# Kernel optimization log

Measured on AMD Instinct MI355X. Metric: run time of the kernel, lower is better.

## Reference

```python
import jax, jax.numpy as jnp
import numpy as np

EMBED_DIM = 1024
NUM_HEADS = 16
HEAD_DIM = EMBED_DIM // NUM_HEADS


def setup_inputs() -> dict:
    key = jax.random.key(0)
    k1, k2, k3, k4 = jax.random.split(key, 4)
    B, T, C = 4, 2048, EMBED_DIM
    scale = 1.0 / np.sqrt(C)
    x = jax.random.normal(k1, (B, T, C), dtype=jnp.float32)
    # nn.Linear(C, 3C, bias=False): weight [3C, C]
    w_qkv = jax.random.normal(k2, (3 * C, C), dtype=jnp.float32) * scale
    # nn.Linear(C, C) with bias
    w_out = jax.random.normal(k3, (C, C), dtype=jnp.float32) * scale
    b_out = jax.random.normal(k4, (C,), dtype=jnp.float32) * 0.01
    return {"x": x, "w_qkv": w_qkv, "w_out": w_out, "b_out": b_out}


def reference(x, w_qkv, w_out, b_out):
    B, T, C = x.shape
    H, D = NUM_HEADS, HEAD_DIM
    qkv = x @ w_qkv.T                      # [B,T,3C]
    q, k, v = jnp.split(qkv, 3, axis=-1)
    # [B,T,C] -> [B,H,T,D]
    q = q.reshape(B, T, H, D).transpose(0, 2, 1, 3)
    k = k.reshape(B, T, H, D).transpose(0, 2, 1, 3)
    v = v.reshape(B, T, H, D).transpose(0, 2, 1, 3)
    scores = jnp.einsum("bhqd,bhkd->bhqk", q, k) / jnp.sqrt(jnp.float32(D))
    causal = jnp.tril(jnp.ones((T, T), dtype=bool))
    scores = jnp.where(causal, scores, -jnp.inf)
    attn = jax.nn.softmax(scores, axis=-1)  # dropout is identity in eval mode
    out = jnp.einsum("bhqk,bhkd->bhqd", attn, v)
    out = out.transpose(0, 2, 1, 3).reshape(B, T, C)
    return out @ w_out.T + b_out
```

## Files before the change

### kernel.cpp

```cpp
#include <hip/hip_runtime.h>
#include <hip/hip_bf16.h>

typedef __bf16 bf16_t;
typedef __bf16 bf16x4 __attribute__((ext_vector_type(4)));
typedef __bf16 bf16x8 __attribute__((ext_vector_type(8)));
typedef float f32x4 __attribute__((ext_vector_type(4)));

#define MFMA16(a, b, c) __builtin_amdgcn_mfma_f32_16x16x32_bf16(a, b, c, 0, 0, 0)

__device__ __forceinline__ void gld16(const bf16_t* g, bf16_t* l) {
  __builtin_amdgcn_global_load_lds(
      (const __attribute__((address_space(1))) unsigned int*)(const void*)g,
      (__attribute__((address_space(3))) unsigned int*)(void*)l, 16, 0, 0);
}

__global__ __launch_bounds__(256) void cvt_f32_bf16(
    const float* __restrict__ src, bf16_t* __restrict__ dst, long long n) {
  long long i = ((long long)blockIdx.x * 256 + threadIdx.x) * 8;
  const long long stride = (long long)gridDim.x * 256 * 8;
  for (; i < n; i += stride) {
    f32x4 a = *(const f32x4*)(src + i);
    f32x4 b = *(const f32x4*)(src + i + 4);
    bf16x8 r;
#pragma unroll
    for (int e = 0; e < 4; ++e) {
      r[e] = (bf16_t)a[e];
      r[4 + e] = (bf16_t)b[e];
    }
    *(bf16x8*)(dst + i) = r;
  }
}

template <bool WF32, typename TC, bool BIAS>
__global__ __launch_bounds__(256, 2) void gemm_async(
    const bf16_t* __restrict__ A, int lda, const void* __restrict__ Wv,
    const float* __restrict__ bias, TC* __restrict__ C, int ldc,
    int M, int N, int K) {
  constexpr int BST = WF32 ? 40 : 32;
  __shared__ bf16_t As[128 * 32];
  __shared__ bf16_t Bs[128 * BST];

  const int tid = threadIdx.x;
  const int i = tid & 63;
  const int w = tid >> 6;
  const int l16 = tid & 15;
  const int quad = (tid >> 4) & 3;
  const int wm = w & 1;
  const int wn = w >> 1;
  const int m0 = blockIdx.y * 128;
  const int n0 = blockIdx.x * 128;

  const bf16_t* ag = A + (size_t)(m0 + w * 32 + (i >> 2)) * lda + (i & 3) * 8;
  bf16_t* as0 = &As[(w * 32) * 32];
  bf16_t* as1 = &As[(w * 32 + 16) * 32];

  const bf16_t* bg = nullptr;
  bf16_t *bs0 = nullptr, *bs1 = nullptr;
  const float* wfg = nullptr;
  bf16_t* bsw = nullptr;
  if (!WF32) {
    bg = (const bf16_t*)Wv + (size_t)(n0 + w * 32 + (i >> 2)) * K + (i & 3) * 8;
    bs0 = &Bs[(w * 32) * 32];
    bs1 = &Bs[(w * 32 + 16) * 32];
  } else {
    const int srow = tid >> 1;
    const int scol = (tid & 1) * 16;
    wfg = (const float*)Wv + (size_t)(n0 + srow) * K + scol;
    bsw = &Bs[srow * BST + scol];
  }

  f32x4 acc[4][4] = {};

  for (int k0 = 0; k0 < K; k0 += 32) {
    __syncthreads();
    gld16(ag + k0, as0);
    gld16(ag + 16 * lda + k0, as1);
    if (!WF32) {
      gld16(bg + k0, bs0);
      gld16(bg + 16 * K + k0, bs1);
    } else {
      f32x4 a = *(const f32x4*)(wfg + k0);
      f32x4 b = *(const f32x4*)(wfg + k0 + 4);
      f32x4 c2 = *(const f32x4*)(wfg + k0 + 8);
      f32x4 d = *(const f32x4*)(wfg + k0 + 12);
      bf16x8 r0, r1;
#pragma unroll
      for (int e = 0; e < 4; ++e) {
        r0[e] = (bf16_t)a[e];
        r0[4 + e] = (bf16_t)b[e];
        r1[e] = (bf16_t)c2[e];
        r1[4 + e] = (bf16_t)d[e];
      }
      *(bf16x8*)(bsw) = r0;
      *(bf16x8*)(bsw + 8) = r1;
    }
    __syncthreads();

    bf16x8 af[4], bfr[4];
#pragma unroll
    for (int t = 0; t < 4; ++t) {
      af[t] = *(const bf16x8*)&As[(wm * 64 + t * 16 + l16) * 32 + quad * 8];
      bfr[t] = *(const bf16x8*)&Bs[(wn * 64 + t * 16 + l16) * BST + quad * 8];
    }
#pragma unroll
    for (int mi = 0; mi < 4; ++mi)
#pragma unroll
      for (int ni = 0; ni < 4; ++ni)
        acc[mi][ni] = MFMA16(af[mi], bfr[ni], acc[mi][ni]);
  }

#pragma unroll
  for (int ni = 0; ni < 4; ++ni) {
    const int col = n0 + wn * 64 + ni * 16 + l16;
    const float bv = BIAS ? bias[col] : 0.0f;
#pragma unroll
    for (int mi = 0; mi < 4; ++mi) {
      const int row = m0 + wm * 64 + mi * 16 + quad * 4;
#pragma unroll
      for (int r = 0; r < 4; ++r)
        C[(size_t)(row + r) * ldc + col] = (TC)(acc[mi][ni][r] + bv);
    }
  }
}

__global__ __launch_bounds__(512, 4) void attn_mfma(bf16_t* __restrict__ qkv) {
  constexpr int T = 2048, C3 = 3072, C = 1024;
  __shared__ bf16_t Ks[64 * 72];
  __shared__ bf16_t Vt[64 * 72];
  __shared__ bf16_t Ps[8 * 16 * 72];

  const int tid = threadIdx.x;
  const int wave = tid >> 6;
  const int lane = tid & 63;
  const int l16 = tid & 15;
  const int quad = (tid >> 4) & 3;
  const int p = blockIdx.x;
  const int b = blockIdx.y >> 4;
  const int h = blockIdx.y & 15;
  bf16_t* base = qkv + (size_t)b * T * C3;

  const int kst = tid >> 2;
  const int ksd = (tid & 3) * 16;
  const int vtok = lane;
  const int vdg = (wave - 4) * 16;

  bf16_t* pw = &Ps[wave * 16 * 72];

  bf16x8 st0, st1;

  for (int s = 0; s < 2; ++s) {
    const int qt = (s == 0) ? p : 15 - p;
    const int Q0 = qt * 128;
    const int qlo = Q0 + wave * 16;
    const int jmax = Q0 + 64;

    bf16x8 qf[2];
    {
      const bf16_t* qp = base + (size_t)(qlo + l16) * C3 + h * 64 + quad * 8;
      bf16x8 a = *(const bf16x8*)qp;
      bf16x8 c = *(const bf16x8*)(qp + 32);
#pragma unroll
      for (int e = 0; e < 8; ++e) {
        a[e] = (bf16_t)((float)a[e] * 0.125f);
        c[e] = (bf16_t)((float)c[e] * 0.125f);
      }
      qf[0] = a;
      qf[1] = c;
    }

    f32x4 Of[4] = {};
    float mrow = -1e30f;
    float lrow = 0.f;

    if (wave < 4) {
      const bf16_t* kp = base + (size_t)kst * C3 + C + h * 64 + ksd;
      st0 = *(const bf16x8*)kp;
      st1 = *(const bf16x8*)(kp + 8);
    } else {
      const bf16_t* vp = base + (size_t)vtok * C3 + 2 * C + h * 64 + vdg;
      st0 = *(const bf16x8*)vp;
      st1 = *(const bf16x8*)(vp + 8);
    }

    for (int j0 = 0; j0 <= jmax; j0 += 64) {
      __syncthreads();
      if (wave < 4) {
        *(bf16x8*)&Ks[kst * 72 + ksd] = st0;
        *(bf16x8*)&Ks[kst * 72 + ksd + 8] = st1;
      } else {
#pragma unroll
        for (int e = 0; e < 8; ++e) {
          Vt[(vdg + e) * 72 + vtok] = st0[e];
          Vt[(vdg + 8 + e) * 72 + vtok] = st1[e];
        }
      }
      if (j0 + 64 <= jmax) {
        const int jn = j0 + 64;
        if (wave < 4) {
          const bf16_t* kp = base + (size_t)(jn + kst) * C3 + C + h * 64 + ksd;
          st0 = *(const bf16x8*)kp;
          st1 = *(const bf16x8*)(kp + 8);
        } else {
          const bf16_t* vp =
              base + (size_t)(jn + vtok) * C3 + 2 * C + h * 64 + vdg;
          st0 = *(const bf16x8*)vp;
          st1 = *(const bf16x8*)(vp + 8);
        }
      }
      __syncthreads();

      if (qlo + 15 < j0) continue;

      float Sv[4][4];
      const int qrow = qlo + l16;
      __builtin_amdgcn_s_setprio(1);
#pragma unroll
      for (int nt = 0; nt < 4; ++nt) {
        f32x4 sacc = {};
#pragma unroll
        for (int s2 = 0; s2 < 2; ++s2) {
          bf16x8 kf =
              *(const bf16x8*)&Ks[(nt * 16 + l16) * 72 + s2 * 32 + quad * 8];
          sacc = MFMA16(kf, qf[s2], sacc);
        }
        const int keyb = j0 + nt * 16 + quad * 4;
#pragma unroll
        for (int r = 0; r < 4; ++r)
          Sv[nt][r] = (keyb + r > qrow) ? -1e30f : sacc[r];
      }
      __builtin_amdgcn_s_setprio(0);

      float vm[4];
#pragma unroll
      for (int nt = 0; nt < 4; ++nt)
        vm[nt] = fmaxf(fmaxf(Sv[nt][0], Sv[nt][1]),
                       fmaxf(Sv[nt][2], Sv[nt][3]));
      float v = fmaxf(fmaxf(vm[0], vm[1]), fmaxf(vm[2], vm[3]));
      v = fmaxf(v, __shfl_xor(v, 16));
      v = fmaxf(v, __shfl_xor(v, 32));

      if (__any(v > mrow)) {
        const float mnew = fmaxf(mrow, v);
        const float alpha = __expf(mrow - mnew);
        mrow = mnew;
        lrow *= alpha;
        float ar[4];
#pragma unroll
        for (int r = 0; r < 4; ++r) ar[r] = __shfl(alpha, quad * 4 + r, 16);
#pragma unroll
        for (int dt = 0; dt < 4; ++dt)
#pragma unroll
          for (int r = 0; r < 4; ++r) Of[dt][r] *= ar[r];
      }

      float rsn[4];
#pragma unroll
      for (int nt = 0; nt < 4; ++nt) {
        bf16x4 pk;
        float r0 = __expf(Sv[nt][0] - mrow);
        float r1 = __expf(Sv[nt][1] - mrow);
        float r2 = __expf(Sv[nt][2] - mrow);
        float r3 = __expf(Sv[nt][3] - mrow);
        pk[0] = (bf16_t)r0;
        pk[1] = (bf16_t)r1;
        pk[2] = (bf16_t)r2;
        pk[3] = (bf16_t)r3;
        rsn[nt] = (r0 + r1) + (r2 + r3);
        *(bf16x4*)&pw[l16 * 72 + nt * 16 + quad * 4] = pk;
      }
      float rs = (rsn[0] + rsn[1]) + (rsn[2] + rsn[3]);
      rs += __shfl_xor(rs, 16);
      rs += __shfl_xor(rs, 32);
      lrow += rs;

      bf16x8 pf0 = *(const bf16x8*)&pw[l16 * 72 + quad * 8];
      bf16x8 pf1 = *(const bf16x8*)&pw[l16 * 72 + 32 + quad * 8];
      __builtin_amdgcn_s_setprio(1);
#pragma unroll
      for (int dt = 0; dt < 4; ++dt) {
        bf16x8 vf0 = *(const bf16x8*)&Vt[(dt * 16 + l16) * 72 + quad * 8];
        bf16x8 vf1 = *(const bf16x8*)&Vt[(dt * 16 + l16) * 72 + 32 + quad * 8];
        Of[dt] = MFMA16(pf0, vf0, Of[dt]);
        Of[dt] = MFMA16(pf1, vf1, Of[dt]);
      }
      __builtin_amdgcn_s_setprio(0);
    }

    float lr[4];
#pragma unroll
    for (int r = 0; r < 4; ++r) lr[r] = __shfl(lrow, quad * 4 + r, 16);
    const int t = Q0 + wave * 16 + quad * 4;
#pragma unroll
    for (int r = 0; r < 4; ++r) {
      const float inv = 1.0f / lr[r];
      bf16_t* op = base + (size_t)(t + r) * C3 + h * 64 + l16;
#pragma unroll
      for (int dt = 0; dt < 4; ++dt)
        op[dt * 16] = (bf16_t)(Of[dt][r] * inv);
    }
  }
}

extern "C" void kernel_launch(void* const* d_in, const int* in_sizes, int n_in,
                              void* d_out, int out_size, void* d_ws,
                              size_t ws_size, hipStream_t stream) {
  constexpr int B = 4, T = 2048, C = 1024;
  constexpr int M = B * T;

  const float* x = (const float*)d_in[0];
  const float* w_qkv = (const float*)d_in[1];
  const float* w_out = (const float*)d_in[2];
  const float* b_out = (const float*)d_in[3];
  for (int i = 0; i < n_in; ++i) {
    const long long s = in_sizes[i];
    if (s == (long long)M * C) x = (const float*)d_in[i];
    else if (s == (long long)3 * C * C) w_qkv = (const float*)d_in[i];
    else if (s == (long long)C * C) w_out = (const float*)d_in[i];
    else if (s == C) b_out = (const float*)d_in[i];
  }

  bf16_t* xb = (bf16_t*)d_out;
  bf16_t* wqb = xb + (size_t)M * C;
  bf16_t* qkv = (bf16_t*)d_ws;

  cvt_f32_bf16<<<1024, 256, 0, stream>>>(x, xb, (long long)M * C);
  cvt_f32_bf16<<<512, 256, 0, stream>>>(w_qkv, wqb, 3LL * C * C);

  gemm_async<false, bf16_t, false>
      <<<dim3(3 * C / 128, M / 128), 256, 0, stream>>>(
          xb, C, wqb, nullptr, qkv, 3 * C, M, 3 * C, C);

  attn_mfma<<<dim3(8, B * 16), 512, 0, stream>>>(qkv);

  gemm_async<true, float, true><<<dim3(C / 128, M / 128), 256, 0, stream>>>(
      qkv, 3 * C, w_out, b_out, (float*)d_out, C, M, C, C);
}
```

Before: 286.3 us.

## Use exp2 softmax with folded log2e, skip mask off-diagonal, pre-convert w_out to bf16

```diff
diff --git a/kernel.cpp b/kernel.cpp
--- a/kernel.cpp
+++ b/kernel.cpp
@@ -139,6 +139,8 @@
   const int h = blockIdx.y & 15;
   bf16_t* base = qkv + (size_t)b * T * C3;
 
+  const float QSCALE = 0.125f * 1.44269504088896340736f;
+
   const int kst = tid >> 2;
   const int ksd = (tid & 3) * 16;
   const int vtok = lane;
@@ -161,8 +163,8 @@
       bf16x8 c = *(const bf16x8*)(qp + 32);
 #pragma unroll
       for (int e = 0; e < 8; ++e) {
-        a[e] = (bf16_t)((float)a[e] * 0.125f);
-        c[e] = (bf16_t)((float)c[e] * 0.125f);
+        a[e] = (bf16_t)((float)a[e] * QSCALE);
+        c[e] = (bf16_t)((float)c[e] * QSCALE);
       }
       qf[0] = a;
       qf[1] = c;
@@ -223,12 +225,20 @@
               *(const bf16x8*)&Ks[(nt * 16 + l16) * 72 + s2 * 32 + quad * 8];
           sacc = MFMA16(kf, qf[s2], sacc);
         }
-        const int keyb = j0 + nt * 16 + quad * 4;
-#pragma unroll
-        for (int r = 0; r < 4; ++r)
-          Sv[nt][r] = (keyb + r > qrow) ? -1e30f : sacc[r];
+#pragma unroll
+        for (int r = 0; r < 4; ++r) Sv[nt][r] = sacc[r];
       }
       __builtin_amdgcn_s_setprio(0);
+
+      if (j0 + 64 > qlo) {
+#pragma unroll
+        for (int nt = 0; nt < 4; ++nt) {
+          const int keyb = j0 + nt * 16 + quad * 4;
+#pragma unroll
+          for (int r = 0; r < 4; ++r)
+            if (keyb + r > qrow) Sv[nt][r] = -1e30f;
+        }
+      }
 
       float vm[4];
 #pragma unroll
@@ -241,7 +251,7 @@
 
       if (__any(v > mrow)) {
         const float mnew = fmaxf(mrow, v);
-        const float alpha = __expf(mrow - mnew);
+        const float alpha = __builtin_amdgcn_exp2f(mrow - mnew);
         mrow = mnew;
         lrow *= alpha;
         float ar[4];
@@ -257,10 +267,10 @@
 #pragma unroll
       for (int nt = 0; nt < 4; ++nt) {
         bf16x4 pk;
-        float r0 = __expf(Sv[nt][0] - mrow);
-        float r1 = __expf(Sv[nt][1] - mrow);
-        float r2 = __expf(Sv[nt][2] - mrow);
-        float r3 = __expf(Sv[nt][3] - mrow);
+        float r0 = __builtin_amdgcn_exp2f(Sv[nt][0] - mrow);
+        float r1 = __builtin_amdgcn_exp2f(Sv[nt][1] - mrow);
+        float r2 = __builtin_amdgcn_exp2f(Sv[nt][2] - mrow);
+        float r3 = __builtin_amdgcn_exp2f(Sv[nt][3] - mrow);
         pk[0] = (bf16_t)r0;
         pk[1] = (bf16_t)r1;
         pk[2] = (bf16_t)r2;
@@ -322,9 +332,14 @@
   bf16_t* xb = (bf16_t*)d_out;
   bf16_t* wqb = xb + (size_t)M * C;
   bf16_t* qkv = (bf16_t*)d_ws;
+  bf16_t* wob = qkv + (size_t)M * 3 * C;
+  const bool ws_ok =
+      ws_size >= (size_t)M * 3 * C * 2 + (size_t)C * C * 2;
 
   cvt_f32_bf16<<<1024, 256, 0, stream>>>(x, xb, (long long)M * C);
   cvt_f32_bf16<<<512, 256, 0, stream>>>(w_qkv, wqb, 3LL * C * C);
+  if (ws_ok)
+    cvt_f32_bf16<<<256, 256, 0, stream>>>(w_out, wob, (long long)C * C);
 
   gemm_async<false, bf16_t, false>
       <<<dim3(3 * C / 128, M / 128), 256, 0, stream>>>(
@@ -332,6 +347,10 @@
 
   attn_mfma<<<dim3(8, B * 16), 512, 0, stream>>>(qkv);
 
-  gemm_async<true, float, true><<<dim3(C / 128, M / 128), 256, 0, stream>>>(
-      qkv, 3 * C, w_out, b_out, (float*)d_out, C, M, C, C);
-}
+  if (ws_ok)
+    gemm_async<false, float, true><<<dim3(C / 128, M / 128), 256, 0, stream>>>(
+        qkv, 3 * C, wob, b_out, (float*)d_out, C, M, C, C);
+  else
+    gemm_async<true, float, true><<<dim3(C / 128, M / 128), 256, 0, stream>>>(
+        qkv, 3 * C, w_out, b_out, (float*)d_out, C, M, C, C);
+}
```

After: 265.1 us. 1.08x faster.
